# Kernel tuning notes

Hardware: AMD Instinct MI355X
Metric: run time of the kernel (lower is better)

Reference implementation:

```python
import jax, jax.numpy as jnp
import numpy as np

N = 8192       # num_nodes
DEG = 16       # edges per node
E = N * DEG    # num_edges
F = 128        # num_features
R = 20         # num_rbf_features
L = 3          # num_message_passing_layers
CUT = 3.0      # cutoff_dist


def setup_inputs() -> dict:
    key = jax.random.key(0)
    ks = jax.random.split(key, 18)
    atoms = jax.random.randint(ks[0], (N,), 1, 119)
    # every node appears as a destination exactly DEG times -> bincount > 0
    idx_i = jnp.repeat(jnp.arange(N), DEG)
    idx_j = jax.random.randint(ks[1], (E,), 0, N)
    raw = jax.random.normal(ks[2], (E, 3), jnp.float32)
    rel_dir = raw / jnp.linalg.norm(raw, axis=-1, keepdims=True)
    rel_dist = jax.random.uniform(ks[3], (E,), jnp.float32, 0.1, CUT - 1e-3)
    emb = (jax.random.normal(ks[4], (119, F), jnp.float32) / np.sqrt(F)).at[0].set(0.0)
    def w(k, shape, fan_in):
        return jax.random.normal(k, shape, jnp.float32) / np.sqrt(fan_in)
    return {
        'atoms': atoms, 'idx_i': idx_i, 'idx_j': idx_j,
        'rel_dir': rel_dir, 'rel_dist': rel_dist, 'emb': emb,
        'msg_w1': w(ks[5], (L, F, F), F), 'msg_b1': jnp.zeros((L, F), jnp.float32),
        'msg_w2': w(ks[6], (L, F, 3 * F), F), 'msg_b2': jnp.zeros((L, 3 * F), jnp.float32),
        'rbf_w': w(ks[7], (L, R, 3 * F), R), 'rbf_b': jnp.zeros((L, 3 * F), jnp.float32),
        'Uw': w(ks[8], (L, F, F), F), 'Vw': w(ks[9], (L, F, F), F),
        'upd_w1': w(ks[10], (L, 2 * F, F), 2 * F), 'upd_b1': jnp.zeros((L, F), jnp.float32),
        'upd_w2': w(ks[11], (L, F, 3 * F), F), 'upd_b2': jnp.zeros((L, 3 * F), jnp.float32),
    }


def painn_forward(atoms, idx_i, idx_j, rel_dir, rel_dist, emb,
                  msg_w1, msg_b1, msg_w2, msg_b2, rbf_w, rbf_b,
                  Uw, Vw, upd_w1, upd_b1, upd_w2, upd_b2):
    silu = jax.nn.silu
    # cosine cutoff and sinusoidal RBF features of edge distances
    cut = 0.5 * (jnp.cos(jnp.pi * rel_dist / CUT) + 1.0)               # [E]
    n = jnp.arange(1, R + 1, dtype=rel_dist.dtype)
    rbf = jnp.sin(n * jnp.pi * rel_dist[:, None] / CUT) / rel_dist[:, None]  # [E,R]

    s = emb[atoms]                                   # [N,F]
    v = jnp.zeros((N, F, 3), s.dtype)                # [N,F,3]
    counts = jax.ops.segment_sum(jnp.ones(E, s.dtype), idx_i, num_segments=N)  # bincount

    for l in range(L):
        # ---- message block ----
        phi = silu(s @ msg_w1[l] + msg_b1[l]) @ msg_w2[l] + msg_b2[l]  # [N,3F]
        W = (rbf @ rbf_w[l] + rbf_b[l]) * cut[:, None]                 # [E,3F]
        phi_W = phi[idx_j] * W                                         # [E,3F]
        p_vv, p_ss, p_vs = jnp.split(phi_W, 3, axis=-1)
        ds = jax.ops.segment_sum(p_ss, idx_i, num_segments=N) / counts[:, None]
        ve = v[idx_j] * p_vv[..., None] + p_vs[..., None] * rel_dir[:, None, :]  # [E,F,3]
        dv = jax.ops.segment_sum(ve, idx_i, num_segments=N) / counts[:, None, None]
        s = s + ds
        v = v + dv
        # ---- update block ----
        Uv = jnp.einsum('nfc,fg->ngc', v, Uw[l])       # [N,F,3]
        Vv = jnp.einsum('nfc,fg->ngc', v, Vw[l])       # [N,F,3]
        a_in = jnp.concatenate([jnp.linalg.norm(Vv, axis=-1), s], axis=-1)  # [N,2F]
        a = silu(a_in @ upd_w1[l] + upd_b1[l]) @ upd_w2[l] + upd_b2[l]      # [N,3F]
        a_vv, a_sv, a_ss = jnp.split(a, 3, axis=-1)
        s = s + a_ss + a_sv * jnp.sum(Uv * Vv, axis=-1)
        v = v + Uv * a_vv[..., None]
    return s, v


def reference(atoms, idx_i, idx_j, rel_dir, rel_dist, emb,
              msg_w1, msg_b1, msg_w2, msg_b2, rbf_w, rbf_b,
              Uw, Vw, upd_w1, upd_b1, upd_w2, upd_b2):
    return painn_forward(atoms, idx_i, idx_j, rel_dir, rel_dist, emb,
                         msg_w1, msg_b1, msg_w2, msg_b2, rbf_w, rbf_b,
                         Uw, Vw, upd_w1, upd_b1, upd_w2, upd_b2)
```

## Files before the change

kernel.cpp:

```cpp
#include <hip/hip_runtime.h>
#include <hip/hip_fp16.h>

#define N_NODES 8192
#define DEG     16
#define NEDGE   (N_NODES*DEG)
#define F       128
#define F3      384
#define RBF     20
#define NLAYER  3
#define NF      (N_NODES*F)
#define PI_F    3.14159265358979f

typedef unsigned short u16;
typedef __bf16 bf16x8 __attribute__((ext_vector_type(8)));
typedef float  f32x4  __attribute__((ext_vector_type(4)));
typedef _Float16 f16x2 __attribute__((ext_vector_type(2)));

__device__ __forceinline__ float bf2f(u16 u){ return __uint_as_float(((unsigned)u)<<16); }
__device__ __forceinline__ u16 f2bf(float f){
  unsigned x = __float_as_uint(f);
  unsigned r = (x + 0x7FFFu + ((x>>16)&1u)) >> 16;
  return (u16)r;
}
__device__ __forceinline__ float lo_bf(unsigned u){ return __uint_as_float(u<<16); }
// ... 229 lines not shown
    rw2[1][r2] = rwp2[r2*F3 + F + f];
    rw2[2][r2] = rwp2[r2*F3 + 2*F + f];
  }

  int nA = blockIdx.x * 2;
  if (t < 128) ed4[t] = ed_g[(size_t)nA*64 + t];
  __syncthreads();

  int n = nA + half;
  int base = half*64;
  float ds=0.f, dv0=0.f, dv1=0.f, dv2=0.f;

  int j0 = (int)(ed4[base+3].z & (N_NODES-1));
  uint2    pa = bufA[(size_t)j0*F + f];
  unsigned pb = bufB[(size_t)j0*F + f];
  for (int el=0;el<DEG;el++){
    uint2 cpa = pa; unsigned cpb = pb;
    if (el+1 < DEG){
      int j1 = (int)(ed4[base+(el+1)*4+3].z & (N_NODES-1));
      pa = bufA[(size_t)j1*F + f];
      pb = bufB[(size_t)j1*F + f];
    }
    uint4 q0 = ed4[base+el*4+0];
    uint4 q1 = ed4[base+el*4+1];
    uint4 q2 = ed4[base+el*4+2];
    uint4 q3 = ed4[base+el*4+3];
    unsigned rc[11] = {q0.x,q0.y,q0.z,q0.w, q1.x,q1.y,q1.z,q1.w, q2.x,q2.y,q2.z};
    float Wvv = 0.f, Wss = 0.f, Wvs = 0.f;
    #pragma unroll
    for (int r2=0;r2<11;r2++){
      Wvv = fdot2u(rc[r2], rw2[0][r2], Wvv);
      Wss = fdot2u(rc[r2], rw2[1][r2], Wss);
      Wvs = fdot2u(rc[r2], rw2[2][r2], Wvs);
    }
    float pvv = Wvv*lo_bf(cpa.x), pss = Wss*hi_bf(cpa.x), pvs = Wvs*lo_bf(cpb);
    ds += pss;
    dv0 += lo_bf(cpa.y)*pvv + pvs*__uint_as_float(q2.w);
    dv1 += hi_bf(cpa.y)*pvv + pvs*__uint_as_float(q3.x);
    dv2 += hi_bf(cpb)  *pvv + pvs*__uint_as_float(q3.y);
  }
  size_t i = (size_t)n*F + f;
  const float inv = 1.f/DEG;
  float sv = s[i] + ds*inv;
  s[i] = sv;
  { u16 hb = f2bf(sv); s_h[i] = hb; s_l[i] = f2bf(sv - bf2f(hb)); }
  float o0 = bf2f(vi_h[i])              + bf2f(vi_l[i])              + dv0*inv;
  float o1 = bf2f(vi_h[NF+i])           + bf2f(vi_l[NF+i])           + dv1*inv;
  float o2 = bf2f(vi_h[2*(size_t)NF+i]) + bf2f(vi_l[2*(size_t)NF+i]) + dv2*inv;
  u16 h0=f2bf(o0), h1=f2bf(o1), h2=f2bf(o2);
  vo_h[i]=h0; vo_h[NF+i]=h1; vo_h[2*(size_t)NF+i]=h2;
  vo_l[i]=f2bf(o0-bf2f(h0)); vo_l[NF+i]=f2bf(o1-bf2f(h1)); vo_l[2*(size_t)NF+i]=f2bf(o2-bf2f(h2));
}

__global__ __launch_bounds__(512) void k_fused(
    const u16* __restrict__ uvh,  const u16* __restrict__ uvl,
    const u16* __restrict__ w1h_, const u16* __restrict__ w1l_,
    const u16* __restrict__ w2h_, const u16* __restrict__ w2l_,
    const float* __restrict__ b1, const float* __restrict__ b2,
    const u16* __restrict__ mw1h_, const u16* __restrict__ mw1l_,
    const u16* __restrict__ mw2h_, const u16* __restrict__ mw2l_,
    const float* __restrict__ mb1, const float* __restrict__ mb2,
    float* __restrict__ s, u16* __restrict__ s_h, u16* __restrict__ s_l,
    u16* __restrict__ v_h, u16* __restrict__ v_l,
    u16* __restrict__ bufA16, u16* __restrict__ bufB16,
    float* __restrict__ out){
  __shared__ __align__(16) u16 AV [6*32*136];
  __shared__ __align__(16) u16 Bt [2*64*136];
  __shared__ __align__(16) u16 AIb[2*32*264];
  __shared__ __align__(16) u16 Hx [2*32*136];
  int t = threadIdx.x;
  int lane = t&63, w = t>>6;
  int qr = (w>>2)<<4;
  int qw = w&3;
  int l15 = lane&15, q8 = (lane>>4)<<3, qrow = (lane>>4)<<2;
  int row0 = blockIdx.x<<5;

  #pragma unroll
  for (int q=0;q<6;q++){
    int id = t + 512*q;
    int chl = id>>9, rem = id&511, r = rem>>4, c8 = (rem&15)<<3;
    const u16* src = ((chl&1)? v_l : v_h) + (size_t)(chl>>1)*NF + (size_t)(row0+r)*F + c8;
    *(uint4*)&AV[((size_t)chl*32 + r)*136 + c8] = *(const uint4*)src;
  }
  #pragma unroll
  for (int q=0;q<2;q++){
    int id = t + 512*q;
    int hl = id>>9, rem = id&511, r = rem>>4, c8 = (rem&15)<<3;
    const u16* src = (hl? s_l : s_h) + (size_t)(row0+r)*F + c8;
    *(uint4*)&AIb[(size_t)hl*32*264 + r*264 + 128 + c8] = *(const uint4*)src;
  }

  f32x4 aU[2][3], aV[2][3];
  #pragma unroll
  for (int cg=0; cg<4; cg++){
    __syncthreads();
    #pragma unroll
    for (int q=0;q<4;q++){
      int id = t + 512*q;
      int hl = id>>10, rem = id&1023, r = rem>>4, c8 = (rem&15)<<3;
      const u16* src = (hl? uvl : uvh) + (size_t)(cg*64+r)*F + c8;
      *(uint4*)&Bt[(size_t)hl*64*136 + r*136 + c8] = *(const uint4*)src;
    }
    __syncthreads();
    #pragma unroll
    for (int c=0;c<3;c++){
      f32x4 acc; acc[0]=0;acc[1]=0;acc[2]=0;acc[3]=0;
      #pragma unroll
      for (int k0=0;k0<F;k0+=32){
        bf16x8 a_h = *(const bf16x8*)&AV[((2*c  )*32 + qr + l15)*136 + k0 + q8];
        bf16x8 a_l = *(const bf16x8*)&AV[((2*c+1)*32 + qr + l15)*136 + k0 + q8];
        bf16x8 b_h = *(const bf16x8*)&Bt[(qw*16+l15)*136 + k0 + q8];
        bf16x8 b_l = *(const bf16x8*)&Bt[64*136 + (qw*16+l15)*136 + k0 + q8];
        acc = __builtin_amdgcn_mfma_f32_16x16x32_bf16(a_h, b_h, acc, 0,0,0);
        acc = __builtin_amdgcn_mfma_f32_16x16x32_bf16(a_h, b_l, acc, 0,0,0);
        acc = __builtin_amdgcn_mfma_f32_16x16x32_bf16(a_l, b_h, acc, 0,0,0);
      }
      if (cg<2) aU[cg][c]=acc; else aV[cg-2][c]=acc;
    }
  }

  f32x4 dotf[2];
  #pragma unroll
  for (int g=0; g<2; g++){
    #pragma unroll
    for (int r=0;r<4;r++){
      float d=0.f, n2=0.f;
      #pragma unroll
      for (int c=0;c<3;c++){ d += aU[g][c][r]*aV[g][c][r]; n2 += aV[g][c][r]*aV[g][c][r]; }
      dotf[g][r]=d;
      int row = qr+qrow+r, col = g*64+qw*16+l15;
      float vn = sqrtf(n2);
      u16 h = f2bf(vn);
      AIb[row*264+col] = h;
      AIb[32*264 + row*264+col] = f2bf(vn - bf2f(h));
    }
  }

  #pragma unroll
  for (int cgc=0; cgc<2; cgc++){
    f32x4 acc; acc[0]=0;acc[1]=0;acc[2]=0;acc[3]=0;
    #pragma unroll
    for (int kc=0; kc<2; kc++){
      __syncthreads();
      #pragma unroll
      for (int q=0;q<4;q++){
        int id = t + 512*q;
        int hl = id>>10, rem = id&1023, r = rem>>4, c8 = (rem&15)<<3;
        const u16* src = (hl? w1l_ : w1h_) + (size_t)(cgc*64+r)*256 + kc*128 + c8;
        *(uint4*)&Bt[(size_t)hl*64*136 + r*136 + c8] = *(const uint4*)src;
      }
      __syncthreads();
      #pragma unroll
      for (int ks=0; ks<128; ks+=32){
        bf16x8 a_h = *(const bf16x8*)&AIb[(qr+l15)*264 + kc*128 + ks + q8];
        bf16x8 a_l = *(const bf16x8*)&AIb[32*264 + (qr+l15)*264 + kc*128 + ks + q8];
        bf16x8 b_h = *(const bf16x8*)&Bt[(qw*16+l15)*136 + ks + q8];
        bf16x8 b_l = *(const bf16x8*)&Bt[64*136 + (qw*16+l15)*136 + ks + q8];
        acc = __builtin_amdgcn_mfma_f32_16x16x32_bf16(a_h, b_h, acc, 0,0,0);
        acc = __builtin_amdgcn_mfma_f32_16x16x32_bf16(a_h, b_l, acc, 0,0,0);
        acc = __builtin_amdgcn_mfma_f32_16x16x32_bf16(a_l, b_h, acc, 0,0,0);
      }
    }
    int col = cgc*64 + qw*16 + l15;
    float bb = b1[col];
    #pragma unroll
    for (int r=0;r<4;r++){
      float val = silu_f(acc[r] + bb);
      u16 hb = f2bf(val);
      Hx[(qr+qrow+r)*136 + col] = hb;
      Hx[32*136 + (qr+qrow+r)*136 + col] = f2bf(val - bf2f(hb));
    }
  }

  __half* aL = (__half*)AIb;
  #pragma unroll
  for (int cg=0; cg<6; cg++){
    __syncthreads();
    #pragma unroll
    for (int q=0;q<4;q++){
      int id = t + 512*q;
      int hl = id>>10, rem = id&1023, r = rem>>4, c8 = (rem&15)<<3;
      const u16* src = (hl? w2l_ : w2h_) + (size_t)(cg*64+r)*F + c8;
      *(uint4*)&Bt[(size_t)hl*64*136 + r*136 + c8] = *(const uint4*)src;
    }
    __syncthreads();
    f32x4 acc; acc[0]=0;acc[1]=0;acc[2]=0;acc[3]=0;
    #pragma unroll
    for (int k0=0;k0<F;k0+=32){
      bf16x8 a_h = *(const bf16x8*)&Hx[(qr+l15)*136 + k0 + q8];
      bf16x8 a_l = *(const bf16x8*)&Hx[32*136 + (qr+l15)*136 + k0 + q8];
      bf16x8 b_h = *(const bf16x8*)&Bt[(qw*16+l15)*136 + k0 + q8];
      bf16x8 b_l = *(const bf16x8*)&Bt[64*136 + (qw*16+l15)*136 + k0 + q8];
      acc = __builtin_amdgcn_mfma_f32_16x16x32_bf16(a_h, b_h, acc, 0,0,0);
      acc = __builtin_amdgcn_mfma_f32_16x16x32_bf16(a_h, b_l, acc, 0,0,0);
      acc = __builtin_amdgcn_mfma_f32_16x16x32_bf16(a_l, b_h, acc, 0,0,0);
    }
    int gc = cg*64 + qw*16 + l15;
    float bb = b2[gc];
    #pragma unroll
    for (int r=0;r<4;r++)
      aL[(qr+qrow+r)*392 + gc] = __float2half(acc[r] + bb);
  }
  __syncthreads();

  bool domsg = (mw1h_ != nullptr);
  #pragma unroll
  for (int g=0; g<2; g++){
    #pragma unroll
    for (int r=0; r<4; r++){
      int row = qr+qrow+r;
      int col = g*64+qw*16+l15;
      int grow = row0+row;
      size_t i = (size_t)grow*F + col;
      float avv = __half2float(aL[row*392 + col]);
      float asv = __half2float(aL[row*392 + F + col]);
      float ass = __half2float(aL[row*392 + 2*F + col]);
      float sv = s[i] + ass + asv*dotf[g][r];
      s[i] = sv;
      u16 hb = f2bf(sv); u16 lb = f2bf(sv - bf2f(hb));
      s_h[i]=hb; s_l[i]=lb;
      float nv[3];
      #pragma unroll
      for (int c=0;c<3;c++){
        float vold = bf2f(AV[((2*c)*32+row)*136+col]) + bf2f(AV[((2*c+1)*32+row)*136+col]);
        nv[c] = vold + aU[g][c][r]*avv;
      }
      u16 h0=f2bf(nv[0]), h1=f2bf(nv[1]), h2=f2bf(nv[2]);
      v_h[i]=h0; v_h[NF+i]=h1; v_h[2*(size_t)NF+i]=h2;
      v_l[i]=f2bf(nv[0]-bf2f(h0)); v_l[NF+i]=f2bf(nv[1]-bf2f(h1)); v_l[2*(size_t)NF+i]=f2bf(nv[2]-bf2f(h2));
      bufA16[i*4+2]=h0; bufA16[i*4+3]=h1; bufB16[i*2+1]=h2;
      if (out){
        out[i] = sv;
        out[NF + i*3 + 0] = nv[0];
        out[NF + i*3 + 1] = nv[1];
        out[NF + i*3 + 2] = nv[2];
      }
      if (domsg){
        Hx[row*136+col] = hb;
        Hx[32*136 + row*136+col] = lb;
      }
    }
  }

  if (domsg){
    #pragma unroll
    for (int cgc=0; cgc<2; cgc++){
      __syncthreads();
      #pragma unroll
      for (int q=0;q<4;q++){
        int id = t + 512*q;
        int hl = id>>10, rem = id&1023, r = rem>>4, c8 = (rem&15)<<3;
        const u16* src = (hl? mw1l_ : mw1h_) + (size_t)(cgc*64+r)*F + c8;
        *(uint4*)&Bt[(size_t)hl*64*136 + r*136 + c8] = *(const uint4*)src;
      }
      __syncthreads();
      f32x4 acc; acc[0]=0;acc[1]=0;acc[2]=0;acc[3]=0;
      #pragma unroll
      for (int k0=0;k0<F;k0+=32){
        bf16x8 a_h = *(const bf16x8*)&Hx[(qr+l15)*136 + k0 + q8];
        bf16x8 a_l = *(const bf16x8*)&Hx[32*136 + (qr+l15)*136 + k0 + q8];
        bf16x8 b_h = *(const bf16x8*)&Bt[(qw*16+l15)*136 + k0 + q8];
        bf16x8 b_l = *(const bf16x8*)&Bt[64*136 + (qw*16+l15)*136 + k0 + q8];
        acc = __builtin_amdgcn_mfma_f32_16x16x32_bf16(a_h, b_h, acc, 0,0,0);
        acc = __builtin_amdgcn_mfma_f32_16x16x32_bf16(a_h, b_l, acc, 0,0,0);
        acc = __builtin_amdgcn_mfma_f32_16x16x32_bf16(a_l, b_h, acc, 0,0,0);
      }
      int col = cgc*64 + qw*16 + l15;
      float bb = mb1[col];
      #pragma unroll
      for (int r=0;r<4;r++){
        float val = silu_f(acc[r] + bb);
        u16 hb = f2bf(val);
        AIb[(qr+qrow+r)*136 + col] = hb;
        AIb[32*136 + (qr+qrow+r)*136 + col] = f2bf(val - bf2f(hb));
      }
    }
    #pragma unroll
    for (int cg=0; cg<6; cg++){
      __syncthreads();
      #pragma unroll
      for (int q=0;q<4;q++){
        int id = t + 512*q;
        int hl = id>>10, rem = id&1023, r = rem>>4, c8 = (rem&15)<<3;
        const u16* src = (hl? mw2l_ : mw2h_) + (size_t)(cg*64+r)*F + c8;
        *(uint4*)&Bt[(size_t)hl*64*136 + r*136 + c8] = *(const uint4*)src;
      }
      __syncthreads();
      f32x4 acc; acc[0]=0;acc[1]=0;acc[2]=0;acc[3]=0;
      #pragma unroll
      for (int k0=0;k0<F;k0+=32){
        bf16x8 a_h = *(const bf16x8*)&AIb[(qr+l15)*136 + k0 + q8];
        bf16x8 a_l = *(const bf16x8*)&AIb[32*136 + (qr+l15)*136 + k0 + q8];
        bf16x8 b_h = *(const bf16x8*)&Bt[(qw*16+l15)*136 + k0 + q8];
        bf16x8 b_l = *(const bf16x8*)&Bt[64*136 + (qw*16+l15)*136 + k0 + q8];
        acc = __builtin_amdgcn_mfma_f32_16x16x32_bf16(a_h, b_h, acc, 0,0,0);
        acc = __builtin_amdgcn_mfma_f32_16x16x32_bf16(a_h, b_l, acc, 0,0,0);
        acc = __builtin_amdgcn_mfma_f32_16x16x32_bf16(a_l, b_h, acc, 0,0,0);
      }
      int gc = cg*64 + qw*16 + l15;
      float bb = mb2[gc];
      #pragma unroll
      for (int r=0;r<4;r++){
        int grow = row0 + qr + qrow + r;
        u16 v16 = f2bf(acc[r] + bb);
        size_t rowo = (size_t)grow*F;
        if (gc < F)        bufA16[(rowo + gc)*4 + 0]     = v16;
        else if (gc < 2*F) bufA16[(rowo + gc - F)*4 + 1] = v16;
        else               bufB16[(rowo + gc - 2*F)*2]   = v16;
      }
    }
  }
}

extern "C" void kernel_launch(void* const* d_in, const int* in_sizes, int n_in,
                              void* d_out, int out_size, void* d_ws, size_t ws_size,
                              hipStream_t stream) {
  const int* atoms   = (const int*)d_in[0];
  const int* idxj    = (const int*)d_in[2];

  float* W = (float*)d_ws;
  size_t off = 64;
  int* flag = (int*)d_ws;
  #define ALLOCF(name, cnt) float* name = W+off; off += (((cnt)+63)&~(size_t)63)
  #define ALLOCU(name, cnt) u16* name = (u16*)(W+off); off += ((((cnt)+1)/2+63)&~(size_t)63)
  ALLOCF(c_mb1, NLAYER*F);
  ALLOCF(c_mb2, NLAYER*F3);
  ALLOCF(c_b1,  NLAYER*F);
  ALLOCF(c_b2,  NLAYER*F3);
  unsigned* c_rwp2 = (unsigned*)(W+off); off += ((NLAYER*11*F3+63)&~(size_t)63);
  uint4* edata = (uint4*)(W+off); off += (size_t)NEDGE*16;
  ALLOCU(w_mw1h, NLAYER*F*F);   ALLOCU(w_mw1l, NLAYER*F*F);
  ALLOCU(w_mw2h, NLAYER*F*F3);  ALLOCU(w_mw2l, NLAYER*F*F3);
  ALLOCU(w_uvh,  NLAYER*256*F); ALLOCU(w_uvl,  NLAYER*256*F);
  ALLOCU(w_w1h,  NLAYER*F*256); ALLOCU(w_w1l,  NLAYER*F*256);
  ALLOCU(w_w2h,  NLAYER*F*F3);  ALLOCU(w_w2l,  NLAYER*F*F3);
  uint2* bufA = (uint2*)(W+off); off += (size_t)2*NF;
  unsigned* bufB = (unsigned*)(W+off); off += (size_t)NF;
  ALLOCU(p0h, (size_t)3*NF); ALLOCU(p0l, (size_t)3*NF);
  ALLOCU(p1h, (size_t)3*NF); ALLOCU(p1l, (size_t)3*NF);
  ALLOCU(s_h,  NF); ALLOCU(s_l,  NF);
  ALLOCF(s,    NF);

  k_detect<<<1, 64, 0, stream>>>((const u16*)d_in[4], flag);
  k_prep<<<(PREP_TOTAL+255)/256, 256, 0, stream>>>(
      d_in[7], d_in[9], d_in[15], d_in[17],
      d_in[10], d_in[11],
      d_in[6], d_in[8], d_in[14], d_in[16],
      d_in[12], d_in[13],
      d_in[4], d_in[3], idxj,
      atoms, d_in[5],
      c_mb1, c_mb2, c_b1, c_b2, c_rwp2,
      w_mw1h, w_mw1l, w_mw2h, w_mw2l, w_w1h, w_w1l,
      w_w2h, w_w2l, w_uvh, w_uvl, edata,
      s, s_h, s_l, p0h, p0l, (u16*)bufA, (u16*)bufB, flag);

  k_msg<<<N_NODES/16, 256, 0, stream>>>(
      s_h, s_l,
      w_mw1h, w_mw1l, w_mw2h, w_mw2l,
      c_mb1, c_mb2,
      (u16*)bufA, (u16*)bufB);

  for (int l=0; l<NLAYER; l++){
    u16* vih = (l & 1) ? p1h : p0h;
    u16* vil = (l & 1) ? p1l : p0l;
// ... 24 lines not shown
```

Measured before the change: 340.7 us.

## Prefetch weight tiles into registers across all GEMM stages of fused update kernel

Replaces the per-tile global-load-then-store into shared memory with a register prefetch pipeline that runs through all the weight tiles of the fused update/message kernel. The next tile is loaded while MFMAs run on the current one. It also hoists the A-operand fragments into registers, reorders loops so each B fragment is reused across three accumulators, and sets launch bounds to two blocks per SM. This hides global weight-load latency behind compute, at the cost of extra registers that may cause spills under the tighter occupancy bound.

```diff
diff --git a/kernel.cpp b/kernel.cpp
--- a/kernel.cpp
+++ b/kernel.cpp
@@ -305,7 +305,35 @@
   vo_l[i]=f2bf(o0-bf2f(h0)); vo_l[NF+i]=f2bf(o1-bf2f(h1)); vo_l[2*(size_t)NF+i]=f2bf(o2-bf2f(h2));
 }
 
-__global__ __launch_bounds__(512) void k_fused(
+__device__ __forceinline__ void load_tile(int idx, int t,
+    const u16* uvh, const u16* uvl,
+    const u16* w1h_, const u16* w1l_,
+    const u16* w2h_, const u16* w2l_,
+    const u16* mw1h_, const u16* mw1l_,
+    const u16* mw2h_, const u16* mw2l_,
+    uint4 pre[4]){
+  const u16 *bh, *bl; int st, off;
+  if (idx < 4){       bh=uvh;   bl=uvl;   st=128; off = idx*(64*128); }
+  else if (idx < 8){  int r2=idx-4;
+                      bh=w1h_;  bl=w1l_;  st=256; off = (r2&1)*(64*256) + (r2>>1)*128; }
+  else if (idx < 14){ bh=w2h_;  bl=w2l_;  st=128; off = (idx-8)*(64*128); }
+  else if (idx < 16){ bh=mw1h_; bl=mw1l_; st=128; off = (idx-14)*(64*128); }
+  else {              bh=mw2h_; bl=mw2l_; st=128; off = (idx-16)*(64*128); }
+  #pragma unroll
+  for (int q=0;q<4;q++){
+    int id = t + 512*q; int hl = id>>10, rem = id&1023, r = rem>>4, c8 = (rem&15)<<3;
+    pre[q] = *(const uint4*)((hl?bl:bh) + (size_t)off + r*st + c8);
+  }
+}
+__device__ __forceinline__ void write_tile(u16* Bt, int t, const uint4 pre[4]){
+  #pragma unroll
+  for (int q=0;q<4;q++){
+    int id = t + 512*q; int hl = id>>10, rem = id&1023, r = rem>>4, c8 = (rem&15)<<3;
+    *(uint4*)(Bt + hl*(64*136) + r*136 + c8) = pre[q];
+  }
+}
+
+__global__ __launch_bounds__(512, 2) void k_fused(
     const u16* __restrict__ uvh,  const u16* __restrict__ uvl,
     const u16* __restrict__ w1h_, const u16* __restrict__ w1l_,
     const u16* __restrict__ w2h_, const u16* __restrict__ w2l_,
@@ -327,6 +355,8 @@
   int qw = w&3;
   int l15 = lane&15, q8 = (lane>>4)<<3, qrow = (lane>>4)<<2;
   int row0 = blockIdx.x<<5;
+  bool domsg = (mw1h_ != nullptr);
+  const int NT = domsg ? 22 : 14;
 
   #pragma unroll
   for (int q=0;q<6;q++){
@@ -343,32 +373,35 @@
     *(uint4*)&AIb[(size_t)hl*32*264 + r*264 + 128 + c8] = *(const uint4*)src;
   }
 
+  uint4 pre[4];
+  load_tile(0, t, uvh,uvl, w1h_,w1l_, w2h_,w2l_, mw1h_,mw1l_, mw2h_,mw2l_, pre);
+
   f32x4 aU[2][3], aV[2][3];
   #pragma unroll
   for (int cg=0; cg<4; cg++){
     __syncthreads();
-    #pragma unroll
-    for (int q=0;q<4;q++){
-      int id = t + 512*q;
-      int hl = id>>10, rem = id&1023, r = rem>>4, c8 = (rem&15)<<3;
-      const u16* src = (hl? uvl : uvh) + (size_t)(cg*64+r)*F + c8;
-      *(uint4*)&Bt[(size_t)hl*64*136 + r*136 + c8] = *(const uint4*)src;
-    }
-    __syncthreads();
-    #pragma unroll
-    for (int c=0;c<3;c++){
-      f32x4 acc; acc[0]=0;acc[1]=0;acc[2]=0;acc[3]=0;
-      #pragma unroll
-      for (int k0=0;k0<F;k0+=32){
+    write_tile(Bt, t, pre);
+    __syncthreads();
+    load_tile(cg+1, t, uvh,uvl, w1h_,w1l_, w2h_,w2l_, mw1h_,mw1l_, mw2h_,mw2l_, pre);
+    f32x4 acc3[3];
+    #pragma unroll
+    for (int c=0;c<3;c++){ acc3[c][0]=0; acc3[c][1]=0; acc3[c][2]=0; acc3[c][3]=0; }
+    #pragma unroll
+    for (int k0=0;k0<F;k0+=32){
+      bf16x8 b_h = *(const bf16x8*)&Bt[(qw*16+l15)*136 + k0 + q8];
+      bf16x8 b_l = *(const bf16x8*)&Bt[64*136 + (qw*16+l15)*136 + k0 + q8];
+      #pragma unroll
+      for (int c=0;c<3;c++){
         bf16x8 a_h = *(const bf16x8*)&AV[((2*c  )*32 + qr + l15)*136 + k0 + q8];
         bf16x8 a_l = *(const bf16x8*)&AV[((2*c+1)*32 + qr + l15)*136 + k0 + q8];
-        bf16x8 b_h = *(const bf16x8*)&Bt[(qw*16+l15)*136 + k0 + q8];
-        bf16x8 b_l = *(const bf16x8*)&Bt[64*136 + (qw*16+l15)*136 + k0 + q8];
-        acc = __builtin_amdgcn_mfma_f32_16x16x32_bf16(a_h, b_h, acc, 0,0,0);
-        acc = __builtin_amdgcn_mfma_f32_16x16x32_bf16(a_h, b_l, acc, 0,0,0);
-        acc = __builtin_amdgcn_mfma_f32_16x16x32_bf16(a_l, b_h, acc, 0,0,0);
-      }
-      if (cg<2) aU[cg][c]=acc; else aV[cg-2][c]=acc;
+        acc3[c] = __builtin_amdgcn_mfma_f32_16x16x32_bf16(a_h, b_h, acc3[c], 0,0,0);
+        acc3[c] = __builtin_amdgcn_mfma_f32_16x16x32_bf16(a_h, b_l, acc3[c], 0,0,0);
+        acc3[c] = __builtin_amdgcn_mfma_f32_16x16x32_bf16(a_l, b_h, acc3[c], 0,0,0);
+      }
+    }
+    #pragma unroll
+    for (int c=0;c<3;c++){
+      if (cg<2) aU[cg][c]=acc3[c]; else aV[cg-2][c]=acc3[c];
     }
   }
 
@@ -388,65 +421,72 @@
       AIb[32*264 + row*264+col] = f2bf(vn - bf2f(h));
     }
   }
-
+  __syncthreads();
+
+  f32x4 acc2[2];
+  acc2[0][0]=0;acc2[0][1]=0;acc2[0][2]=0;acc2[0][3]=0; acc2[1]=acc2[0];
+  #pragma unroll
+  for (int kc=0; kc<2; kc++){
+    bf16x8 a2h[4], a2l[4];
+    #pragma unroll
+    for (int ks=0; ks<4; ks++){
+      a2h[ks] = *(const bf16x8*)&AIb[(qr+l15)*264 + kc*128 + ks*32 + q8];
+      a2l[ks] = *(const bf16x8*)&AIb[32*264 + (qr+l15)*264 + kc*128 + ks*32 + q8];
+    }
+    #pragma unroll
+    for (int cgc=0; cgc<2; cgc++){
+      int tix = 4 + kc*2 + cgc;
+      __syncthreads();
+      write_tile(Bt, t, pre);
+      __syncthreads();
+      load_tile(tix+1, t, uvh,uvl, w1h_,w1l_, w2h_,w2l_, mw1h_,mw1l_, mw2h_,mw2l_, pre);
+      #pragma unroll
+      for (int ks=0; ks<4; ks++){
+        bf16x8 b_h = *(const bf16x8*)&Bt[(qw*16+l15)*136 + ks*32 + q8];
+        bf16x8 b_l = *(const bf16x8*)&Bt[64*136 + (qw*16+l15)*136 + ks*32 + q8];
+        acc2[cgc] = __builtin_amdgcn_mfma_f32_16x16x32_bf16(a2h[ks], b_h, acc2[cgc], 0,0,0);
+        acc2[cgc] = __builtin_amdgcn_mfma_f32_16x16x32_bf16(a2h[ks], b_l, acc2[cgc], 0,0,0);
+        acc2[cgc] = __builtin_amdgcn_mfma_f32_16x16x32_bf16(a2l[ks], b_h, acc2[cgc], 0,0,0);
+      }
+    }
+  }
   #pragma unroll
   for (int cgc=0; cgc<2; cgc++){
-    f32x4 acc; acc[0]=0;acc[1]=0;acc[2]=0;acc[3]=0;
-    #pragma unroll
-    for (int kc=0; kc<2; kc++){
-      __syncthreads();
-      #pragma unroll
-      for (int q=0;q<4;q++){
-        int id = t + 512*q;
-        int hl = id>>10, rem = id&1023, r = rem>>4, c8 = (rem&15)<<3;
-        const u16* src = (hl? w1l_ : w1h_) + (size_t)(cgc*64+r)*256 + kc*128 + c8;
-        *(uint4*)&Bt[(size_t)hl*64*136 + r*136 + c8] = *(const uint4*)src;
-      }
-      __syncthreads();
-      #pragma unroll
-      for (int ks=0; ks<128; ks+=32){
-        bf16x8 a_h = *(const bf16x8*)&AIb[(qr+l15)*264 + kc*128 + ks + q8];
-        bf16x8 a_l = *(const bf16x8*)&AIb[32*264 + (qr+l15)*264 + kc*128 + ks + q8];
-        bf16x8 b_h = *(const bf16x8*)&Bt[(qw*16+l15)*136 + ks + q8];
-        bf16x8 b_l = *(const bf16x8*)&Bt[64*136 + (qw*16+l15)*136 + ks + q8];
-        acc = __builtin_amdgcn_mfma_f32_16x16x32_bf16(a_h, b_h, acc, 0,0,0);
-        acc = __builtin_amdgcn_mfma_f32_16x16x32_bf16(a_h, b_l, acc, 0,0,0);
-        acc = __builtin_amdgcn_mfma_f32_16x16x32_bf16(a_l, b_h, acc, 0,0,0);
-      }
-    }
     int col = cgc*64 + qw*16 + l15;
     float bb = b1[col];
     #pragma unroll
     for (int r=0;r<4;r++){
-      float val = silu_f(acc[r] + bb);
+      float val = silu_f(acc2[cgc][r] + bb);
       u16 hb = f2bf(val);
       Hx[(qr+qrow+r)*136 + col] = hb;
       Hx[32*136 + (qr+qrow+r)*136 + col] = f2bf(val - bf2f(hb));
     }
   }
-
+  __syncthreads();
+
+  bf16x8 hah[4], hal[4];
+  #pragma unroll
+  for (int ks=0; ks<4; ks++){
+    hah[ks] = *(const bf16x8*)&Hx[(qr+l15)*136 + ks*32 + q8];
+    hal[ks] = *(const bf16x8*)&Hx[32*136 + (qr+l15)*136 + ks*32 + q8];
+  }
   __half* aL = (__half*)AIb;
   #pragma unroll
   for (int cg=0; cg<6; cg++){
-    __syncthreads();
-    #pragma unroll
-    for (int q=0;q<4;q++){
-      int id = t + 512*q;
-      int hl = id>>10, rem = id&1023, r = rem>>4, c8 = (rem&15)<<3;
-      const u16* src = (hl? w2l_ : w2h_) + (size_t)(cg*64+r)*F + c8;
-      *(uint4*)&Bt[(size_t)hl*64*136 + r*136 + c8] = *(const uint4*)src;
-    }
-    __syncthreads();
+    int tix = 8 + cg;
+    __syncthreads();
+    write_tile(Bt, t, pre);
+    __syncthreads();
+    if (tix+1 < NT)
+      load_tile(tix+1, t, uvh,uvl, w1h_,w1l_, w2h_,w2l_, mw1h_,mw1l_, mw2h_,mw2l_, pre);
     f32x4 acc; acc[0]=0;acc[1]=0;acc[2]=0;acc[3]=0;
     #pragma unroll
-    for (int k0=0;k0<F;k0+=32){
-      bf16x8 a_h = *(const bf16x8*)&Hx[(qr+l15)*136 + k0 + q8];
-      bf16x8 a_l = *(const bf16x8*)&Hx[32*136 + (qr+l15)*136 + k0 + q8];
-      bf16x8 b_h = *(const bf16x8*)&Bt[(qw*16+l15)*136 + k0 + q8];
-      bf16x8 b_l = *(const bf16x8*)&Bt[64*136 + (qw*16+l15)*136 + k0 + q8];
-      acc = __builtin_amdgcn_mfma_f32_16x16x32_bf16(a_h, b_h, acc, 0,0,0);
-      acc = __builtin_amdgcn_mfma_f32_16x16x32_bf16(a_h, b_l, acc, 0,0,0);
-      acc = __builtin_amdgcn_mfma_f32_16x16x32_bf16(a_l, b_h, acc, 0,0,0);
+    for (int ks=0; ks<4; ks++){
+      bf16x8 b_h = *(const bf16x8*)&Bt[(qw*16+l15)*136 + ks*32 + q8];
+      bf16x8 b_l = *(const bf16x8*)&Bt[64*136 + (qw*16+l15)*136 + ks*32 + q8];
+      acc = __builtin_amdgcn_mfma_f32_16x16x32_bf16(hah[ks], b_h, acc, 0,0,0);
+      acc = __builtin_amdgcn_mfma_f32_16x16x32_bf16(hah[ks], b_l, acc, 0,0,0);
+      acc = __builtin_amdgcn_mfma_f32_16x16x32_bf16(hal[ks], b_h, acc, 0,0,0);
     }
     int gc = cg*64 + qw*16 + l15;
     float bb = b2[gc];
@@ -456,7 +496,6 @@
   }
   __syncthreads();
 
-  bool domsg = (mw1h_ != nullptr);
   #pragma unroll
   for (int g=0; g<2; g++){
     #pragma unroll
@@ -496,59 +535,67 @@
   }
 
   if (domsg){
+    __syncthreads();
+    bf16x8 sah[4], sal[4];
+    #pragma unroll
+    for (int ks=0; ks<4; ks++){
+      sah[ks] = *(const bf16x8*)&Hx[(qr+l15)*136 + ks*32 + q8];
+      sal[ks] = *(const bf16x8*)&Hx[32*136 + (qr+l15)*136 + ks*32 + q8];
+    }
+    f32x4 acc4[2];
+    acc4[0][0]=0;acc4[0][1]=0;acc4[0][2]=0;acc4[0][3]=0; acc4[1]=acc4[0];
     #pragma unroll
     for (int cgc=0; cgc<2; cgc++){
+      int tix = 14 + cgc;
       __syncthreads();
-      #pragma unroll
-      for (int q=0;q<4;q++){
-        int id = t + 512*q;
-        int hl = id>>10, rem = id&1023, r = rem>>4, c8 = (rem&15)<<3;
-        const u16* src = (hl? mw1l_ : mw1h_) + (size_t)(cgc*64+r)*F + c8;
-        *(uint4*)&Bt[(size_t)hl*64*136 + r*136 + c8] = *(const uint4*)src;
-      }
+      write_tile(Bt, t, pre);
       __syncthreads();
-      f32x4 acc; acc[0]=0;acc[1]=0;acc[2]=0;acc[3]=0;
-      #pragma unroll
-      for (int k0=0;k0<F;k0+=32){
-        bf16x8 a_h = *(const bf16x8*)&Hx[(qr+l15)*136 + k0 + q8];
-        bf16x8 a_l = *(const bf16x8*)&Hx[32*136 + (qr+l15)*136 + k0 + q8];
-        bf16x8 b_h = *(const bf16x8*)&Bt[(qw*16+l15)*136 + k0 + q8];
-        bf16x8 b_l = *(const bf16x8*)&Bt[64*136 + (qw*16+l15)*136 + k0 + q8];
-        acc = __builtin_amdgcn_mfma_f32_16x16x32_bf16(a_h, b_h, acc, 0,0,0);
-        acc = __builtin_amdgcn_mfma_f32_16x16x32_bf16(a_h, b_l, acc, 0,0,0);
-        acc = __builtin_amdgcn_mfma_f32_16x16x32_bf16(a_l, b_h, acc, 0,0,0);
-      }
+      load_tile(tix+1, t, uvh,uvl, w1h_,w1l_, w2h_,w2l_, mw1h_,mw1l_, mw2h_,mw2l_, pre);
+      #pragma unroll
+      for (int ks=0; ks<4; ks++){
+        bf16x8 b_h = *(const bf16x8*)&Bt[(qw*16+l15)*136 + ks*32 + q8];
+        bf16x8 b_l = *(const bf16x8*)&Bt[64*136 + (qw*16+l15)*136 + ks*32 + q8];
+        acc4[cgc] = __builtin_amdgcn_mfma_f32_16x16x32_bf16(sah[ks], b_h, acc4[cgc], 0,0,0);
+        acc4[cgc] = __builtin_amdgcn_mfma_f32_16x16x32_bf16(sah[ks], b_l, acc4[cgc], 0,0,0);
+        acc4[cgc] = __builtin_amdgcn_mfma_f32_16x16x32_bf16(sal[ks], b_h, acc4[cgc], 0,0,0);
+      }
+    }
+    #pragma unroll
+    for (int cgc=0; cgc<2; cgc++){
       int col = cgc*64 + qw*16 + l15;
       float bb = mb1[col];
       #pragma unroll
       for (int r=0;r<4;r++){
-        float val = silu_f(acc[r] + bb);
+        float val = silu_f(acc4[cgc][r] + bb);
         u16 hb = f2bf(val);
         AIb[(qr+qrow+r)*136 + col] = hb;
         AIb[32*136 + (qr+qrow+r)*136 + col] = f2bf(val - bf2f(hb));
       }
     }
+    __syncthreads();
+
+    bf16x8 mhh[4], mhl[4];
+    #pragma unroll
+    for (int ks=0; ks<4; ks++){
+      mhh[ks] = *(const bf16x8*)&AIb[(qr+l15)*136 + ks*32 + q8];
+      mhl[ks] = *(const bf16x8*)&AIb[32*136 + (qr+l15)*136 + ks*32 + q8];
+    }
     #pragma unroll
     for (int cg=0; cg<6; cg++){
+      int tix = 16 + cg;
       __syncthreads();
-      #pragma unroll
-      for (int q=0;q<4;q++){
-        int id = t + 512*q;
-        int hl = id>>10, rem = id&1023, r = rem>>4, c8 = (rem&15)<<3;
-        const u16* src = (hl? mw2l_ : mw2h_) + (size_t)(cg*64+r)*F + c8;
-        *(uint4*)&Bt[(size_t)hl*64*136 + r*136 + c8] = *(const uint4*)src;
-      }
+      write_tile(Bt, t, pre);
       __syncthreads();
+      if (tix+1 < NT)
+        load_tile(tix+1, t, uvh,uvl, w1h_,w1l_, w2h_,w2l_, mw1h_,mw1l_, mw2h_,mw2l_, pre);
       f32x4 acc; acc[0]=0;acc[1]=0;acc[2]=0;acc[3]=0;
       #pragma unroll
-      for (int k0=0;k0<F;k0+=32){
-        bf16x8 a_h = *(const bf16x8*)&AIb[(qr+l15)*136 + k0 + q8];
-        bf16x8 a_l = *(const bf16x8*)&AIb[32*136 + (qr+l15)*136 + k0 + q8];
-        bf16x8 b_h = *(const bf16x8*)&Bt[(qw*16+l15)*136 + k0 + q8];
-        bf16x8 b_l = *(const bf16x8*)&Bt[64*136 + (qw*16+l15)*136 + k0 + q8];
-        acc = __builtin_amdgcn_mfma_f32_16x16x32_bf16(a_h, b_h, acc, 0,0,0);
-        acc = __builtin_amdgcn_mfma_f32_16x16x32_bf16(a_h, b_l, acc, 0,0,0);
-        acc = __builtin_amdgcn_mfma_f32_16x16x32_bf16(a_l, b_h, acc, 0,0,0);
+      for (int ks=0; ks<4; ks++){
+        bf16x8 b_h = *(const bf16x8*)&Bt[(qw*16+l15)*136 + ks*32 + q8];
+        bf16x8 b_l = *(const bf16x8*)&Bt[64*136 + (qw*16+l15)*136 + ks*32 + q8];
+        acc = __builtin_amdgcn_mfma_f32_16x16x32_bf16(mhh[ks], b_h, acc, 0,0,0);
+        acc = __builtin_amdgcn_mfma_f32_16x16x32_bf16(mhh[ks], b_l, acc, 0,0,0);
+        acc = __builtin_amdgcn_mfma_f32_16x16x32_bf16(mhl[ks], b_h, acc, 0,0,0);
       }
       int gc = cg*64 + qw*16 + l15;
       float bb = mb2[gc];
```

Measured after the change: 408.7 us. 20.0% more time.

## Software-pipeline weight tile loads in fused update kernel via register prefetch

Applied to the files above, without the earlier changes.

Weight tiles for all GEMM stages in the fused update/message kernel are now prefetched into registers one step ahead. The next tile's global load overlaps the current tile's MFMA work, and the LDS write happens at the following barrier. A-operand fragments are hoisted into registers and reused across output column groups. The first-layer GEMM loop is reordered so each B tile read feeds three accumulators. This costs more registers per thread and extra barriers around the A-fragment loads.

```diff
diff --git a/kernel.cpp b/kernel.cpp
--- a/kernel.cpp
+++ b/kernel.cpp
@@ -305,6 +305,44 @@
   vo_l[i]=f2bf(o0-bf2f(h0)); vo_l[NF+i]=f2bf(o1-bf2f(h1)); vo_l[2*(size_t)NF+i]=f2bf(o2-bf2f(h2));
 }
 
+struct Pre4 { uint4 v0, v1, v2, v3; };
+
+__device__ __forceinline__ Pre4 load_tile(int idx, int t,
+    const u16* uvh, const u16* uvl,
+    const u16* w1h_, const u16* w1l_,
+    const u16* w2h_, const u16* w2l_,
+    const u16* mw1h_, const u16* mw1l_,
+    const u16* mw2h_, const u16* mw2l_){
+  const u16 *bh, *bl; int st, off;
+  if (idx < 4){       bh=uvh;   bl=uvl;   st=128; off = idx*(64*128); }
+  else if (idx < 8){  int r2=idx-4;
+                      bh=w1h_;  bl=w1l_;  st=256; off = (r2&1)*(64*256) + (r2>>1)*128; }
+  else if (idx < 14){ bh=w2h_;  bl=w2l_;  st=128; off = (idx-8)*(64*128); }
+  else if (idx < 16){ bh=mw1h_; bl=mw1l_; st=128; off = (idx-14)*(64*128); }
+  else {              bh=mw2h_; bl=mw2l_; st=128; off = (idx-16)*(64*128); }
+  Pre4 p;
+  { int id=t;      int hl=id>>10, rem=id&1023, r=rem>>4, c8=(rem&15)<<3;
+    p.v0 = *(const uint4*)((hl?bl:bh) + (size_t)off + r*st + c8); }
+  { int id=t+512;  int hl=id>>10, rem=id&1023, r=rem>>4, c8=(rem&15)<<3;
+    p.v1 = *(const uint4*)((hl?bl:bh) + (size_t)off + r*st + c8); }
+  { int id=t+1024; int hl=id>>10, rem=id&1023, r=rem>>4, c8=(rem&15)<<3;
+    p.v2 = *(const uint4*)((hl?bl:bh) + (size_t)off + r*st + c8); }
+  { int id=t+1536; int hl=id>>10, rem=id&1023, r=rem>>4, c8=(rem&15)<<3;
+    p.v3 = *(const uint4*)((hl?bl:bh) + (size_t)off + r*st + c8); }
+  return p;
+}
+__device__ __forceinline__ void write_tile(u16* Bt, int t, Pre4 p){
+  { int id=t;      int hl=id>>10, rem=id&1023, r=rem>>4, c8=(rem&15)<<3;
+    *(uint4*)(Bt + hl*(64*136) + r*136 + c8) = p.v0; }
+  { int id=t+512;  int hl=id>>10, rem=id&1023, r=rem>>4, c8=(rem&15)<<3;
+    *(uint4*)(Bt + hl*(64*136) + r*136 + c8) = p.v1; }
+  { int id=t+1024; int hl=id>>10, rem=id&1023, r=rem>>4, c8=(rem&15)<<3;
+    *(uint4*)(Bt + hl*(64*136) + r*136 + c8) = p.v2; }
+  { int id=t+1536; int hl=id>>10, rem=id&1023, r=rem>>4, c8=(rem&15)<<3;
+    *(uint4*)(Bt + hl*(64*136) + r*136 + c8) = p.v3; }
+}
+#define TSRC uvh,uvl,w1h_,w1l_,w2h_,w2l_,mw1h_,mw1l_,mw2h_,mw2l_
+
 __global__ __launch_bounds__(512) void k_fused(
     const u16* __restrict__ uvh,  const u16* __restrict__ uvl,
     const u16* __restrict__ w1h_, const u16* __restrict__ w1l_,
@@ -327,6 +365,15 @@
   int qw = w&3;
   int l15 = lane&15, q8 = (lane>>4)<<3, qrow = (lane>>4)<<2;
   int row0 = blockIdx.x<<5;
+  bool domsg = (mw1h_ != nullptr);
+  const int NT = domsg ? 22 : 14;
+
+#define MFMA_STEP(ACC, KS, AH, AL) { \
+    bf16x8 _bh = *(const bf16x8*)&Bt[(qw*16+l15)*136 + (KS)*32 + q8]; \
+    bf16x8 _bl = *(const bf16x8*)&Bt[64*136 + (qw*16+l15)*136 + (KS)*32 + q8]; \
+    ACC = __builtin_amdgcn_mfma_f32_16x16x32_bf16(AH, _bh, ACC, 0,0,0); \
+    ACC = __builtin_amdgcn_mfma_f32_16x16x32_bf16(AH, _bl, ACC, 0,0,0); \
+    ACC = __builtin_amdgcn_mfma_f32_16x16x32_bf16(AL, _bh, ACC, 0,0,0); }
 
   #pragma unroll
   for (int q=0;q<6;q++){
@@ -343,33 +390,45 @@
     *(uint4*)&AIb[(size_t)hl*32*264 + r*264 + 128 + c8] = *(const uint4*)src;
   }
 
+  Pre4 pre = load_tile(0, t, TSRC);
+
   f32x4 aU[2][3], aV[2][3];
   #pragma unroll
   for (int cg=0; cg<4; cg++){
     __syncthreads();
-    #pragma unroll
-    for (int q=0;q<4;q++){
-      int id = t + 512*q;
-      int hl = id>>10, rem = id&1023, r = rem>>4, c8 = (rem&15)<<3;
-      const u16* src = (hl? uvl : uvh) + (size_t)(cg*64+r)*F + c8;
-      *(uint4*)&Bt[(size_t)hl*64*136 + r*136 + c8] = *(const uint4*)src;
-    }
-    __syncthreads();
-    #pragma unroll
-    for (int c=0;c<3;c++){
-      f32x4 acc; acc[0]=0;acc[1]=0;acc[2]=0;acc[3]=0;
-      #pragma unroll
-      for (int k0=0;k0<F;k0+=32){
-        bf16x8 a_h = *(const bf16x8*)&AV[((2*c  )*32 + qr + l15)*136 + k0 + q8];
-        bf16x8 a_l = *(const bf16x8*)&AV[((2*c+1)*32 + qr + l15)*136 + k0 + q8];
-        bf16x8 b_h = *(const bf16x8*)&Bt[(qw*16+l15)*136 + k0 + q8];
-        bf16x8 b_l = *(const bf16x8*)&Bt[64*136 + (qw*16+l15)*136 + k0 + q8];
-        acc = __builtin_amdgcn_mfma_f32_16x16x32_bf16(a_h, b_h, acc, 0,0,0);
-        acc = __builtin_amdgcn_mfma_f32_16x16x32_bf16(a_h, b_l, acc, 0,0,0);
-        acc = __builtin_amdgcn_mfma_f32_16x16x32_bf16(a_l, b_h, acc, 0,0,0);
+    write_tile(Bt, t, pre);
+    __syncthreads();
+    pre = load_tile(cg+1, t, TSRC);
+    f32x4 ac0, ac1, ac2;
+    ac0[0]=0;ac0[1]=0;ac0[2]=0;ac0[3]=0; ac1=ac0; ac2=ac0;
+    #pragma unroll
+    for (int k0=0;k0<F;k0+=32){
+      bf16x8 b_h = *(const bf16x8*)&Bt[(qw*16+l15)*136 + k0 + q8];
+      bf16x8 b_l = *(const bf16x8*)&Bt[64*136 + (qw*16+l15)*136 + k0 + q8];
+      {
+        bf16x8 a_h = *(const bf16x8*)&AV[(0*32 + qr + l15)*136 + k0 + q8];
+        bf16x8 a_l = *(const bf16x8*)&AV[(1*32 + qr + l15)*136 + k0 + q8];
+        ac0 = __builtin_amdgcn_mfma_f32_16x16x32_bf16(a_h, b_h, ac0, 0,0,0);
+        ac0 = __builtin_amdgcn_mfma_f32_16x16x32_bf16(a_h, b_l, ac0, 0,0,0);
+        ac0 = __builtin_amdgcn_mfma_f32_16x16x32_bf16(a_l, b_h, ac0, 0,0,0);
       }
-      if (cg<2) aU[cg][c]=acc; else aV[cg-2][c]=acc;
-    }
+      {
+        bf16x8 a_h = *(const bf16x8*)&AV[(2*32 + qr + l15)*136 + k0 + q8];
+        bf16x8 a_l = *(const bf16x8*)&AV[(3*32 + qr + l15)*136 + k0 + q8];
+        ac1 = __builtin_amdgcn_mfma_f32_16x16x32_bf16(a_h, b_h, ac1, 0,0,0);
+        ac1 = __builtin_amdgcn_mfma_f32_16x16x32_bf16(a_h, b_l, ac1, 0,0,0);
+        ac1 = __builtin_amdgcn_mfma_f32_16x16x32_bf16(a_l, b_h, ac1, 0,0,0);
+      }
+      {
+        bf16x8 a_h = *(const bf16x8*)&AV[(4*32 + qr + l15)*136 + k0 + q8];
+        bf16x8 a_l = *(const bf16x8*)&AV[(5*32 + qr + l15)*136 + k0 + q8];
+        ac2 = __builtin_amdgcn_mfma_f32_16x16x32_bf16(a_h, b_h, ac2, 0,0,0);
+        ac2 = __builtin_amdgcn_mfma_f32_16x16x32_bf16(a_h, b_l, ac2, 0,0,0);
+        ac2 = __builtin_amdgcn_mfma_f32_16x16x32_bf16(a_l, b_h, ac2, 0,0,0);
+      }
+    }
+    if (cg<2){ aU[cg][0]=ac0; aU[cg][1]=ac1; aU[cg][2]=ac2; }
+    else     { aV[cg-2][0]=ac0; aV[cg-2][1]=ac1; aV[cg-2][2]=ac2; }
   }
 
   f32x4 dotf[2];
@@ -388,66 +447,76 @@
       AIb[32*264 + row*264+col] = f2bf(vn - bf2f(h));
     }
   }
-
-  #pragma unroll
-  for (int cgc=0; cgc<2; cgc++){
+  __syncthreads();
+
+  f32x4 acc2A, acc2B;
+  acc2A[0]=0;acc2A[1]=0;acc2A[2]=0;acc2A[3]=0; acc2B=acc2A;
+  #pragma unroll
+  for (int kc=0; kc<2; kc++){
+    const int ab = (qr+l15)*264 + kc*128 + q8;
+    bf16x8 a20h = *(const bf16x8*)&AIb[ab+  0];
+    bf16x8 a21h = *(const bf16x8*)&AIb[ab+ 32];
+    bf16x8 a22h = *(const bf16x8*)&AIb[ab+ 64];
+    bf16x8 a23h = *(const bf16x8*)&AIb[ab+ 96];
+    bf16x8 a20l = *(const bf16x8*)&AIb[32*264+ab+  0];
+    bf16x8 a21l = *(const bf16x8*)&AIb[32*264+ab+ 32];
+    bf16x8 a22l = *(const bf16x8*)&AIb[32*264+ab+ 64];
+    bf16x8 a23l = *(const bf16x8*)&AIb[32*264+ab+ 96];
+    __syncthreads();
+    write_tile(Bt, t, pre);
+    __syncthreads();
+    pre = load_tile(4 + kc*2 + 1, t, TSRC);
+    MFMA_STEP(acc2A, 0, a20h, a20l);
+    MFMA_STEP(acc2A, 1, a21h, a21l);
+    MFMA_STEP(acc2A, 2, a22h, a22l);
+    MFMA_STEP(acc2A, 3, a23h, a23l);
+    __syncthreads();
+    write_tile(Bt, t, pre);
+    __syncthreads();
+    pre = load_tile(4 + kc*2 + 2, t, TSRC);
+    MFMA_STEP(acc2B, 0, a20h, a20l);
+    MFMA_STEP(acc2B, 1, a21h, a21l);
+    MFMA_STEP(acc2B, 2, a22h, a22l);
+    MFMA_STEP(acc2B, 3, a23h, a23l);
+  }
+  {
+    int colA = qw*16 + l15;
+    float bbA = b1[colA], bbB = b1[64+colA];
+    #pragma unroll
+    for (int r=0;r<4;r++){
+      float vA = silu_f(acc2A[r] + bbA);
+      u16 hA = f2bf(vA);
+      Hx[(qr+qrow+r)*136 + colA] = hA;
+      Hx[32*136 + (qr+qrow+r)*136 + colA] = f2bf(vA - bf2f(hA));
+      float vB = silu_f(acc2B[r] + bbB);
+      u16 hB = f2bf(vB);
+      Hx[(qr+qrow+r)*136 + 64+colA] = hB;
+      Hx[32*136 + (qr+qrow+r)*136 + 64+colA] = f2bf(vB - bf2f(hB));
+    }
+  }
+  __syncthreads();
+
+  bf16x8 ha0h = *(const bf16x8*)&Hx[(qr+l15)*136 +  0 + q8];
+  bf16x8 ha1h = *(const bf16x8*)&Hx[(qr+l15)*136 + 32 + q8];
+  bf16x8 ha2h = *(const bf16x8*)&Hx[(qr+l15)*136 + 64 + q8];
+  bf16x8 ha3h = *(const bf16x8*)&Hx[(qr+l15)*136 + 96 + q8];
+  bf16x8 ha0l = *(const bf16x8*)&Hx[32*136 + (qr+l15)*136 +  0 + q8];
+  bf16x8 ha1l = *(const bf16x8*)&Hx[32*136 + (qr+l15)*136 + 32 + q8];
+  bf16x8 ha2l = *(const bf16x8*)&Hx[32*136 + (qr+l15)*136 + 64 + q8];
+  bf16x8 ha3l = *(const bf16x8*)&Hx[32*136 + (qr+l15)*136 + 96 + q8];
+  __half* aL = (__half*)AIb;
+  #pragma unroll
+  for (int cg=0; cg<6; cg++){
+    __syncthreads();
+    write_tile(Bt, t, pre);
+    __syncthreads();
+    if (9+cg < NT)
+      pre = load_tile(9+cg, t, TSRC);
     f32x4 acc; acc[0]=0;acc[1]=0;acc[2]=0;acc[3]=0;
-    #pragma unroll
-    for (int kc=0; kc<2; kc++){
-      __syncthreads();
-      #pragma unroll
-      for (int q=0;q<4;q++){
-        int id = t + 512*q;
-        int hl = id>>10, rem = id&1023, r = rem>>4, c8 = (rem&15)<<3;
-        const u16* src = (hl? w1l_ : w1h_) + (size_t)(cgc*64+r)*256 + kc*128 + c8;
-        *(uint4*)&Bt[(size_t)hl*64*136 + r*136 + c8] = *(const uint4*)src;
-      }
-      __syncthreads();
-      #pragma unroll
-      for (int ks=0; ks<128; ks+=32){
-        bf16x8 a_h = *(const bf16x8*)&AIb[(qr+l15)*264 + kc*128 + ks + q8];
-        bf16x8 a_l = *(const bf16x8*)&AIb[32*264 + (qr+l15)*264 + kc*128 + ks + q8];
-        bf16x8 b_h = *(const bf16x8*)&Bt[(qw*16+l15)*136 + ks + q8];
-        bf16x8 b_l = *(const bf16x8*)&Bt[64*136 + (qw*16+l15)*136 + ks + q8];
-        acc = __builtin_amdgcn_mfma_f32_16x16x32_bf16(a_h, b_h, acc, 0,0,0);
-        acc = __builtin_amdgcn_mfma_f32_16x16x32_bf16(a_h, b_l, acc, 0,0,0);
-        acc = __builtin_amdgcn_mfma_f32_16x16x32_bf16(a_l, b_h, acc, 0,0,0);
-      }
-    }
-    int col = cgc*64 + qw*16 + l15;
-    float bb = b1[col];
-    #pragma unroll
-    for (int r=0;r<4;r++){
-      float val = silu_f(acc[r] + bb);
-      u16 hb = f2bf(val);
-      Hx[(qr+qrow+r)*136 + col] = hb;
-      Hx[32*136 + (qr+qrow+r)*136 + col] = f2bf(val - bf2f(hb));
-    }
-  }
-
-  __half* aL = (__half*)AIb;
-  #pragma unroll
-  for (int cg=0; cg<6; cg++){
-    __syncthreads();
-    #pragma unroll
-    for (int q=0;q<4;q++){
-      int id = t + 512*q;
-      int hl = id>>10, rem = id&1023, r = rem>>4, c8 = (rem&15)<<3;
-      const u16* src = (hl? w2l_ : w2h_) + (size_t)(cg*64+r)*F + c8;
-      *(uint4*)&Bt[(size_t)hl*64*136 + r*136 + c8] = *(const uint4*)src;
-    }
-    __syncthreads();
-    f32x4 acc; acc[0]=0;acc[1]=0;acc[2]=0;acc[3]=0;
-    #pragma unroll
-    for (int k0=0;k0<F;k0+=32){
-      bf16x8 a_h = *(const bf16x8*)&Hx[(qr+l15)*136 + k0 + q8];
-      bf16x8 a_l = *(const bf16x8*)&Hx[32*136 + (qr+l15)*136 + k0 + q8];
-      bf16x8 b_h = *(const bf16x8*)&Bt[(qw*16+l15)*136 + k0 + q8];
-      bf16x8 b_l = *(const bf16x8*)&Bt[64*136 + (qw*16+l15)*136 + k0 + q8];
-      acc = __builtin_amdgcn_mfma_f32_16x16x32_bf16(a_h, b_h, acc, 0,0,0);
-      acc = __builtin_amdgcn_mfma_f32_16x16x32_bf16(a_h, b_l, acc, 0,0,0);
-      acc = __builtin_amdgcn_mfma_f32_16x16x32_bf16(a_l, b_h, acc, 0,0,0);
-    }
+    MFMA_STEP(acc, 0, ha0h, ha0l);
+    MFMA_STEP(acc, 1, ha1h, ha1l);
+    MFMA_STEP(acc, 2, ha2h, ha2l);
+    MFMA_STEP(acc, 3, ha3h, ha3l);
     int gc = cg*64 + qw*16 + l15;
     float bb = b2[gc];
     #pragma unroll
@@ -456,7 +525,6 @@
   }
   __syncthreads();
 
-  bool domsg = (mw1h_ != nullptr);
   #pragma unroll
   for (int g=0; g<2; g++){
     #pragma unroll
@@ -496,60 +564,70 @@
   }
 
   if (domsg){
-    #pragma unroll
-    for (int cgc=0; cgc<2; cgc++){
-      __syncthreads();
-      #pragma unroll
-      for (int q=0;q<4;q++){
-        int id = t + 512*q;
-        int hl = id>>10, rem = id&1023, r = rem>>4, c8 = (rem&15)<<3;
-        const u16* src = (hl? mw1l_ : mw1h_) + (size_t)(cgc*64+r)*F + c8;
-        *(uint4*)&Bt[(size_t)hl*64*136 + r*136 + c8] = *(const uint4*)src;
-      }
-      __syncthreads();
-      f32x4 acc; acc[0]=0;acc[1]=0;acc[2]=0;acc[3]=0;
-      #pragma unroll
-      for (int k0=0;k0<F;k0+=32){
-        bf16x8 a_h = *(const bf16x8*)&Hx[(qr+l15)*136 + k0 + q8];
-        bf16x8 a_l = *(const bf16x8*)&Hx[32*136 + (qr+l15)*136 + k0 + q8];
-        bf16x8 b_h = *(const bf16x8*)&Bt[(qw*16+l15)*136 + k0 + q8];
-        bf16x8 b_l = *(const bf16x8*)&Bt[64*136 + (qw*16+l15)*136 + k0 + q8];
-        acc = __builtin_amdgcn_mfma_f32_16x16x32_bf16(a_h, b_h, acc, 0,0,0);
-        acc = __builtin_amdgcn_mfma_f32_16x16x32_bf16(a_h, b_l, acc, 0,0,0);
-        acc = __builtin_amdgcn_mfma_f32_16x16x32_bf16(a_l, b_h, acc, 0,0,0);
-      }
-      int col = cgc*64 + qw*16 + l15;
-      float bb = mb1[col];
+    __syncthreads();
+    bf16x8 sa0h = *(const bf16x8*)&Hx[(qr+l15)*136 +  0 + q8];
+    bf16x8 sa1h = *(const bf16x8*)&Hx[(qr+l15)*136 + 32 + q8];
+    bf16x8 sa2h = *(const bf16x8*)&Hx[(qr+l15)*136 + 64 + q8];
+    bf16x8 sa3h = *(const bf16x8*)&Hx[(qr+l15)*136 + 96 + q8];
+    bf16x8 sa0l = *(const bf16x8*)&Hx[32*136 + (qr+l15)*136 +  0 + q8];
+    bf16x8 sa1l = *(const bf16x8*)&Hx[32*136 + (qr+l15)*136 + 32 + q8];
+    bf16x8 sa2l = *(const bf16x8*)&Hx[32*136 + (qr+l15)*136 + 64 + q8];
+    bf16x8 sa3l = *(const bf16x8*)&Hx[32*136 + (qr+l15)*136 + 96 + q8];
+    f32x4 acc4A, acc4B;
+    acc4A[0]=0;acc4A[1]=0;acc4A[2]=0;acc4A[3]=0; acc4B=acc4A;
+    __syncthreads();
+    write_tile(Bt, t, pre);
+    __syncthreads();
+    pre = load_tile(15, t, TSRC);
+    MFMA_STEP(acc4A, 0, sa0h, sa0l);
+    MFMA_STEP(acc4A, 1, sa1h, sa1l);
+    MFMA_STEP(acc4A, 2, sa2h, sa2l);
+    MFMA_STEP(acc4A, 3, sa3h, sa3l);
+    __syncthreads();
+    write_tile(Bt, t, pre);
+    __syncthreads();
+    pre = load_tile(16, t, TSRC);
+    MFMA_STEP(acc4B, 0, sa0h, sa0l);
+    MFMA_STEP(acc4B, 1, sa1h, sa1l);
+    MFMA_STEP(acc4B, 2, sa2h, sa2l);
+    MFMA_STEP(acc4B, 3, sa3h, sa3l);
+    {
+      int colA = qw*16 + l15;
+      float bbA = mb1[colA], bbB = mb1[64+colA];
       #pragma unroll
       for (int r=0;r<4;r++){
-        float val = silu_f(acc[r] + bb);
-        u16 hb = f2bf(val);
-        AIb[(qr+qrow+r)*136 + col] = hb;
-        AIb[32*136 + (qr+qrow+r)*136 + col] = f2bf(val - bf2f(hb));
+        float vA = silu_f(acc4A[r] + bbA);
+        u16 hA = f2bf(vA);
+        AIb[(qr+qrow+r)*136 + colA] = hA;
+        AIb[32*136 + (qr+qrow+r)*136 + colA] = f2bf(vA - bf2f(hA));
+        float vB = silu_f(acc4B[r] + bbB);
+        u16 hB = f2bf(vB);
+        AIb[(qr+qrow+r)*136 + 64+colA] = hB;
+        AIb[32*136 + (qr+qrow+r)*136 + 64+colA] = f2bf(vB - bf2f(hB));
       }
     }
+    __syncthreads();
+
+    bf16x8 mh0h = *(const bf16x8*)&AIb[(qr+l15)*136 +  0 + q8];
+    bf16x8 mh1h = *(const bf16x8*)&AIb[(qr+l15)*136 + 32 + q8];
+    bf16x8 mh2h = *(const bf16x8*)&AIb[(qr+l15)*136 + 64 + q8];
+    bf16x8 mh3h = *(const bf16x8*)&AIb[(qr+l15)*136 + 96 + q8];
+    bf16x8 mh0l = *(const bf16x8*)&AIb[32*136 + (qr+l15)*136 +  0 + q8];
+    bf16x8 mh1l = *(const bf16x8*)&AIb[32*136 + (qr+l15)*136 + 32 + q8];
+    bf16x8 mh2l = *(const bf16x8*)&AIb[32*136 + (qr+l15)*136 + 64 + q8];
+    bf16x8 mh3l = *(const bf16x8*)&AIb[32*136 + (qr+l15)*136 + 96 + q8];
     #pragma unroll
     for (int cg=0; cg<6; cg++){
       __syncthreads();
-      #pragma unroll
-      for (int q=0;q<4;q++){
-        int id = t + 512*q;
-        int hl = id>>10, rem = id&1023, r = rem>>4, c8 = (rem&15)<<3;
-        const u16* src = (hl? mw2l_ : mw2h_) + (size_t)(cg*64+r)*F + c8;
-        *(uint4*)&Bt[(size_t)hl*64*136 + r*136 + c8] = *(const uint4*)src;
-      }
+      write_tile(Bt, t, pre);
       __syncthreads();
+      if (17+cg < NT)
+        pre = load_tile(17+cg, t, TSRC);
       f32x4 acc; acc[0]=0;acc[1]=0;acc[2]=0;acc[3]=0;
-      #pragma unroll
-      for (int k0=0;k0<F;k0+=32){
-        bf16x8 a_h = *(const bf16x8*)&AIb[(qr+l15)*136 + k0 + q8];
-        bf16x8 a_l = *(const bf16x8*)&AIb[32*136 + (qr+l15)*136 + k0 + q8];
-        bf16x8 b_h = *(const bf16x8*)&Bt[(qw*16+l15)*136 + k0 + q8];
-        bf16x8 b_l = *(const bf16x8*)&Bt[64*136 + (qw*16+l15)*136 + k0 + q8];
-        acc = __builtin_amdgcn_mfma_f32_16x16x32_bf16(a_h, b_h, acc, 0,0,0);
-        acc = __builtin_amdgcn_mfma_f32_16x16x32_bf16(a_h, b_l, acc, 0,0,0);
-        acc = __builtin_amdgcn_mfma_f32_16x16x32_bf16(a_l, b_h, acc, 0,0,0);
-      }
+      MFMA_STEP(acc, 0, mh0h, mh0l);
+      MFMA_STEP(acc, 1, mh1h, mh1l);
+      MFMA_STEP(acc, 2, mh2h, mh2l);
+      MFMA_STEP(acc, 3, mh3h, mh3l);
       int gc = cg*64 + qw*16 + l15;
       float bb = mb2[gc];
       #pragma unroll
@@ -563,6 +641,7 @@
       }
     }
   }
+#undef MFMA_STEP
 }
 
 extern "C" void kernel_launch(void* const* d_in, const int* in_sizes, int n_in,
```

Result: faster. 319.2 us (-6.3%).
